# Performance work log

Hardware: AMD Instinct MI355X
Metric: run time of the kernel (lower is better)

Reference implementation:

```python
import jax, jax.numpy as jnp
import numpy as np

NEURONS = (3072, 8192, 8192, 10)
TSTEPS = 20
THRES = 1.0
DECAY = (2 ** 4 - 1) / 2 ** 4  # 0.9375


def setup_inputs() -> dict:
    key = jax.random.key(0)
    k_img, k1, k2, k3 = jax.random.split(key, 4)
    image = jax.random.uniform(k_img, (NEURONS[0],), dtype=jnp.float32)
    # He-style init matching torch.randn(neu_in, neu_out) * sqrt(2/neu_in)
    W1 = jax.random.normal(k1, (NEURONS[0], NEURONS[1]), dtype=jnp.float32) * np.sqrt(2 / NEURONS[0])
    W2 = jax.random.normal(k2, (NEURONS[1], NEURONS[2]), dtype=jnp.float32) * np.sqrt(2 / NEURONS[1])
    W3 = jax.random.normal(k3, (NEURONS[2], NEURONS[3]), dtype=jnp.float32) * np.sqrt(2 / NEURONS[2])
    return {"image": image, "W1": W1, "W2": W2, "W3": W3}


def _lif(m, spikes_in, W):
    # integrate: mempot += W.T @ spikes_in
    v = m + spikes_in @ W
    fire = (v >= THRES).astype(v.dtype)
    v = v - THRES * fire
    # leaky decay only where the neuron did not fire
    m_new = v * (fire + (1.0 - fire) * DECAY)
    return m_new, fire


def reference(image, W1, W2, W3):
    f32 = jnp.float32
    init = (
        jnp.zeros(NEURONS[0], f32),  # input membrane
        jnp.zeros(NEURONS[1], f32),  # lin1 membrane
        jnp.zeros(NEURONS[2], f32),  # lin2 membrane
        jnp.zeros(NEURONS[3], f32),  # lin3 membrane
        jnp.zeros(NEURONS[1], f32),  # lin1 spikes from previous step (spikes[t])
        jnp.zeros(NEURONS[2], f32),  # lin2 spikes from previous step
    )

    def step(state, _):
        mi, m1, m2, m3, s1_prev, s2_prev = state
        # input layer: integrate-and-fire, no decay
        mi = mi + image
        s_in = (mi >= THRES).astype(f32)
        mi = mi - THRES * s_in
        # lin1 sees input spikes of the SAME step; lin2/lin3 see previous-step
        # spikes of their pre-layer (pipeline delay in original loop)
        m1, s1 = _lif(m1, s_in, W1)
        m2, s2 = _lif(m2, s1_prev, W2)
        m3, s3 = _lif(m3, s2_prev, W3)
        return (mi, m1, m2, m3, s1, s2), s3

    _, s3_seq = jax.lax.scan(step, init, None, length=TSTEPS)
    # original stores lin3 spikes at indices 1..TSTEPS; index 0 stays zero
    spikes_out = jnp.concatenate([jnp.zeros((1, NEURONS[3]), f32), s3_seq], axis=0)
    return spikes_out
```

## Files before the change

kernel.cpp:

```cpp
#include <hip/hip_runtime.h>

#define TSTEPS 20
#define THRESV 1.0f
#define DECAYV 0.9375f

typedef float f32x4 __attribute__((ext_vector_type(4)));
typedef float f32x2 __attribute__((ext_vector_type(2)));

__device__ float g_sum1[TSTEPS][8192];
__device__ float g_sum2[TSTEPS][8192];
__device__ float g_sum3[TSTEPS][16];

__device__ unsigned g_mask1[3072];
__device__ float g_part1[32][20][8192];
__device__ unsigned g_mask2[8192];
__device__ float g_part2[64][19][8192];


__global__ void snn_input_kernel(const float* __restrict__ image,
                                 unsigned long long* __restrict__ s_in_bits) {
    int i = blockIdx.x * 256 + threadIdx.x;
    float img = image[i];
    float mi = 0.f;
    int word = i >> 6, lane = i & 63;
    for (int t = 0; t < TSTEPS; ++t) {
        mi += img;
        bool fire = (mi >= THRESV);
        if (fire) mi -= THRESV;
        unsigned long long bm = __ballot(fire);
        if (lane == 0) s_in_bits[t * 48 + word] = bm;
    }
}

struct __align__(16) SMem {
    unsigned short list[8192];
    float partials[512];
    unsigned long long bw[128];
    unsigned pc[128];
    int cntp;
};

template <int NW>
__device__ __forceinline__ int compact_par(const unsigned long long* bits, SMem& sm) {
    int tid = threadIdx.x;
    if (tid < NW) {
        unsigned long long w = bits[tid];
        sm.bw[tid] = w;
        sm.pc[tid] = (unsigned)__popcll(w);
    }
    __syncthreads();
    constexpr int WPW = NW / 8;
    int wave = tid >> 6, lane = tid & 63;
    int w0 = wave * WPW;
    int base = 0;
    for (int i = lane; i < w0; i += 64) base += (int)sm.pc[i];
    #pragma unroll
    for (int off = 1; off < 64; off <<= 1) base += __shfl_xor(base, off);
    if (wave == 0) {
        int tot = 0;
        for (int i = lane; i < NW; i += 64) tot += (int)sm.pc[i];
        #pragma unroll
        for (int off = 1; off < 64; off <<= 1) tot += __shfl_xor(tot, off);
        if (lane == 0) sm.cntp = tot;
    }
    for (int i = 0; i < WPW; ++i) {
        unsigned long long w = sm.bw[w0 + i];
        if ((w >> lane) & 1ull) {
            int pos = base + __popcll(w & ((1ull << lane) - 1ull));
            sm.list[pos] = (unsigned short)(((w0 + i) << 6) + lane);
        }
        base += __popcll(w);
    }
    __syncthreads();
    return sm.cntp;
}

#define GLD2(dst, ptr) \
    asm volatile("global_load_dwordx2 %0, %1, off" : "=v"(dst) : "v"(ptr))
#define WAIT8(a0,a1,a2,a3,a4,a5,a6,a7) \
    asm volatile("s_waitcnt vmcnt(0)" \
        : "+v"(a0),"+v"(a1),"+v"(a2),"+v"(a3),"+v"(a4),"+v"(a5),"+v"(a6),"+v"(a7))

__global__ void __launch_bounds__(512)
build_mask1_kernel(const unsigned long long* __restrict__ s_in_bits) {
    int i = blockIdx.x * 512 + threadIdx.x;
    if (i < 3072) {
        unsigned m = 0;
        #pragma unroll
        for (int t = 0; t < 20; ++t)
            m |= (unsigned)((s_in_bits[(size_t)t * 48 + (i >> 6)] >> (i & 63)) & 1ull) << t;
        g_mask1[i] = m;
    }
}

__device__ __forceinline__ void accrow20(f32x2 w, unsigned m, float* ax, float* ay) {
    #pragma unroll
    for (int bb = 0; bb < 20; ++bb)
        if (m & (1u << bb)) { ax[bb] += w.x; ay[bb] += w.y; }
}

__global__ void __launch_bounds__(512)
w1_dense_kernel(const float* __restrict__ W1) {
    __shared__ unsigned msk[96];
    int blk = blockIdx.x;
    int cs = blk >> 5;
    int rb = blk & 31;
    int tid = threadIdx.x;
    if (tid < 96) msk[tid] = g_mask1[rb * 96 + tid];
    __syncthreads();
    int j = cs * 1024 + tid * 2;
    const float* Wp = W1 + (size_t)rb * 96 * 8192 + j;
    float ax[20], ay[20];
    #pragma unroll
    for (int b = 0; b < 20; ++b) { ax[b] = 0.f; ay[b] = 0.f; }
    for (int r = 0; r < 96; r += 8) {
        const float* p = Wp + (size_t)r * 8192;
        f32x2 w0, w1, w2, w3, w4, w5, w6, w7;
        GLD2(w0, p);                GLD2(w1, p + 8192);
        GLD2(w2, p + 2 * 8192);     GLD2(w3, p + 3 * 8192);
        GLD2(w4, p + 4 * 8192);     GLD2(w5, p + 5 * 8192);
        GLD2(w6, p + 6 * 8192);     GLD2(w7, p + 7 * 8192);
        WAIT8(w0, w1, w2, w3, w4, w5, w6, w7);
        accrow20(w0, __builtin_amdgcn_readfirstlane(msk[r    ]), ax, ay);
        accrow20(w1, __builtin_amdgcn_readfirstlane(msk[r + 1]), ax, ay);
        accrow20(w2, __builtin_amdgcn_readfirstlane(msk[r + 2]), ax, ay);
        accrow20(w3, __builtin_amdgcn_readfirstlane(msk[r + 3]), ax, ay);
        accrow20(w4, __builtin_amdgcn_readfirstlane(msk[r + 4]), ax, ay);
        accrow20(w5, __builtin_amdgcn_readfirstlane(msk[r + 5]), ax, ay);
        accrow20(w6, __builtin_amdgcn_readfirstlane(msk[r + 6]), ax, ay);
        accrow20(w7, __builtin_amdgcn_readfirstlane(msk[r + 7]), ax, ay);
    }
    #pragma unroll
    for (int b = 0; b < 20; ++b)
        *(f32x2*)&g_part1[rb][b][j] = (f32x2){ax[b], ay[b]};
}

__global__ void __launch_bounds__(512)
w1_reduce_kernel() {
    int b = blockIdx.x;
    int t = b / 16;
    int j = (b % 16) * 512 + threadIdx.x;
    float s = 0.f;
    #pragma unroll 8
    for (int rb = 0; rb < 32; ++rb)
        s += g_part1[rb][t][j];
    g_sum1[t][j] = s;
}

__global__ void __launch_bounds__(512)
lif_chain_kernel(int which,
                 unsigned long long* __restrict__ bits_out,
                 int tstart) {
    const float* sums = (which == 0) ? &g_sum1[0][0] : &g_sum2[0][0];
    int j = blockIdx.x * 512 + threadIdx.x;
    int lane = threadIdx.x & 63;
    float m = 0.f;
    for (int t = tstart; t < TSTEPS; ++t) {
        float v = m + sums[(size_t)t * 8192 + j];
        bool fire = (v >= THRESV);
        if (fire) v -= THRESV;
        m = fire ? v : v * DECAYV;
        unsigned long long bm = __ballot(fire);
        if (lane == 0) bits_out[(size_t)t * 128 + (j >> 6)] = bm;
    }
}

__global__ void __launch_bounds__(512)
build_mask2_kernel(const unsigned long long* __restrict__ s1_bits) {
    int i = blockIdx.x * 512 + threadIdx.x;
    unsigned m = 0;
    #pragma unroll
    for (int b = 0; b < 19; ++b)
        m |= (unsigned)((s1_bits[(size_t)b * 128 + (i >> 6)] >> (i & 63)) & 1ull) << b;
    g_mask2[i] = m;
}

__device__ __forceinline__ void accrow(f32x2 w, unsigned m, float* ax, float* ay) {
    #pragma unroll
    for (int bb = 0; bb < 19; ++bb)
        if (m & (1u << bb)) { ax[bb] += w.x; ay[bb] += w.y; }
}

__global__ void __launch_bounds__(512)
w2_dense_kernel(const float* __restrict__ W2) {
    __shared__ unsigned msk[128];
    int blk = blockIdx.x;
    int cs = blk >> 6;
    int rb = blk & 63;
    int tid = threadIdx.x;
    if (tid < 128) msk[tid] = g_mask2[rb * 128 + tid];
    __syncthreads();
    int j = cs * 1024 + tid * 2;
    const float* Wp = W2 + (size_t)rb * 128 * 8192 + j;
    float ax[19], ay[19];
    #pragma unroll
    for (int b = 0; b < 19; ++b) { ax[b] = 0.f; ay[b] = 0.f; }
    for (int r = 0; r < 128; r += 8) {
        const float* p = Wp + (size_t)r * 8192;
        f32x2 w0, w1, w2, w3, w4, w5, w6, w7;
        GLD2(w0, p);                GLD2(w1, p + 8192);
        GLD2(w2, p + 2 * 8192);     GLD2(w3, p + 3 * 8192);
        GLD2(w4, p + 4 * 8192);     GLD2(w5, p + 5 * 8192);
        GLD2(w6, p + 6 * 8192);     GLD2(w7, p + 7 * 8192);
        WAIT8(w0, w1, w2, w3, w4, w5, w6, w7);
        accrow(w0, __builtin_amdgcn_readfirstlane(msk[r    ]), ax, ay);
        accrow(w1, __builtin_amdgcn_readfirstlane(msk[r + 1]), ax, ay);
        accrow(w2, __builtin_amdgcn_readfirstlane(msk[r + 2]), ax, ay);
        accrow(w3, __builtin_amdgcn_readfirstlane(msk[r + 3]), ax, ay);
        accrow(w4, __builtin_amdgcn_readfirstlane(msk[r + 4]), ax, ay);
        accrow(w5, __builtin_amdgcn_readfirstlane(msk[r + 5]), ax, ay);
        accrow(w6, __builtin_amdgcn_readfirstlane(msk[r + 6]), ax, ay);
        accrow(w7, __builtin_amdgcn_readfirstlane(msk[r + 7]), ax, ay);
    }
    #pragma unroll
    for (int b = 0; b < 19; ++b)
        *(f32x2*)&g_part2[rb][b][j] = (f32x2){ax[b], ay[b]};
}

__global__ void __launch_bounds__(512)
w2_reduce_kernel() {
    int b = blockIdx.x;
    int t = 1 + b / 16;
    int j = (b % 16) * 512 + threadIdx.x;
    float s = 0.f;
    #pragma unroll 8
    for (int rb = 0; rb < 64; ++rb)
        s += g_part2[rb][t - 1][j];
    g_sum2[t][j] = s;
}

__global__ void __launch_bounds__(512)
w3_sums_kernel(const float* __restrict__ W3,
               const unsigned long long* __restrict__ s2_bits) {
    __shared__ SMem sm;
    int t = blockIdx.x + 1;
    int tid = threadIdx.x;
    int count = compact_par<128>(s2_bits + (size_t)(t - 1) * 128, sm);
    int col = tid & 15, g = tid >> 4;
    float acc = 0.f;
    if (col < 10) {
        for (int k = g; k < count; k += 32)
            acc += W3[(size_t)sm.list[k] * 10 + col];
    }
    sm.partials[g * 16 + col] = acc;
    __syncthreads();
    if (tid < 10) {
        float s = 0.f;
        for (int gg = 0; gg < 32; ++gg) s += sm.partials[gg * 16 + tid];
        g_sum3[t][tid] = s;
    }
}

__global__ void w3_lif_kernel(float* __restrict__ out) {
    int tid = threadIdx.x;
    if (tid < 10) {
        float m = 0.f;
        for (int t = 1; t < TSTEPS; ++t) {
            float v = m + g_sum3[t][tid];
            bool fire = (v >= THRESV);
            if (fire) v -= THRESV;
            m = fire ? v : v * DECAYV;
            out[(t + 1) * 10 + tid] = fire ? 1.f : 0.f;
        }
    }
}

extern "C" void kernel_launch(void* const* d_in, const int* in_sizes, int n_in,
                              void* d_out, int out_size, void* d_ws, size_t ws_size,
                              hipStream_t stream) {
    const float* image = (const float*)d_in[0];
    const float* W1 = (const float*)d_in[1];
    const float* W2 = (const float*)d_in[2];
    const float* W3 = (const float*)d_in[3];
    float* out = (float*)d_out;

    char* ws = (char*)d_ws;
    unsigned long long* s_in_bits = (unsigned long long*)ws;
    unsigned long long* s1_bits = (unsigned long long*)(ws + 7680);
    unsigned long long* s2_bits = (unsigned long long*)(ws + 28160);

    hipMemsetAsync(d_ws, 0, 48640, stream);
    hipMemsetAsync(d_out, 0, (size_t)out_size * sizeof(float), stream);

    snn_input_kernel<<<12, 256, 0, stream>>>(image, s_in_bits);
    build_mask1_kernel<<<6, 512, 0, stream>>>(s_in_bits);
    w1_dense_kernel<<<8 * 32, 512, 0, stream>>>(W1);
    w1_reduce_kernel<<<20 * 16, 512, 0, stream>>>();
    lif_chain_kernel<<<16, 512, 0, stream>>>(0, s1_bits, 0);
    build_mask2_kernel<<<16, 512, 0, stream>>>(s1_bits);
    w2_dense_kernel<<<8 * 64, 512, 0, stream>>>(W2);
    w2_reduce_kernel<<<19 * 16, 512, 0, stream>>>();
    lif_chain_kernel<<<16, 512, 0, stream>>>(1, s2_bits, 1);
    w3_sums_kernel<<<TSTEPS - 1, 512, 0, stream>>>(W3, s2_bits);
    w3_lif_kernel<<<1, 64, 0, stream>>>(out);
}
```

Measured before the change: 177.6 us.

## Fuse mask building and partial reductions into LIF kernels, halve W2 row splits

The input kernel now writes the per-neuron spike masks directly, and the separate mask-building kernels are removed. The partial-sum reductions for layers 1 and 2 are folded into the LIF chain kernels, so the intermediate sum buffers go away. W2 is now split into 32 row blocks of 256 rows each instead of 64 blocks of 128, which halves the partial buffer traffic and halves the blocks launched for the W2 pass. The aim is fewer launches and less global memory traffic. The cost is that the LIF kernels, which run on only 16 blocks, now perform the reductions serially inside the time loop.

New measurement: 242.3 us. +36.4%, slower.

```diff
diff --git a/kernel.cpp b/kernel.cpp
--- a/kernel.cpp
+++ b/kernel.cpp
@@ -4,31 +4,30 @@
 #define THRESV 1.0f
 #define DECAYV 0.9375f
 
-typedef float f32x4 __attribute__((ext_vector_type(4)));
 typedef float f32x2 __attribute__((ext_vector_type(2)));
-
-__device__ float g_sum1[TSTEPS][8192];
-__device__ float g_sum2[TSTEPS][8192];
-__device__ float g_sum3[TSTEPS][16];
 
 __device__ unsigned g_mask1[3072];
 __device__ float g_part1[32][20][8192];
 __device__ unsigned g_mask2[8192];
-__device__ float g_part2[64][19][8192];
-
-
-__global__ void snn_input_kernel(const float* __restrict__ image,
-                                 unsigned long long* __restrict__ s_in_bits) {
-    int i = blockIdx.x * 256 + threadIdx.x;
-    float img = image[i];
-    float mi = 0.f;
-    int word = i >> 6, lane = i & 63;
-    for (int t = 0; t < TSTEPS; ++t) {
-        mi += img;
-        bool fire = (mi >= THRESV);
-        if (fire) mi -= THRESV;
-        unsigned long long bm = __ballot(fire);
-        if (lane == 0) s_in_bits[t * 48 + word] = bm;
+__device__ float g_part2[32][19][8192];
+__device__ float g_sum3[TSTEPS][16];
+
+
+__global__ void __launch_bounds__(512)
+snn_input_kernel(const float* __restrict__ image) {
+    int i = blockIdx.x * 512 + threadIdx.x;
+    if (i < 3072) {
+        float img = image[i];
+        float mi = 0.f;
+        unsigned mask = 0;
+        #pragma unroll
+        for (int t = 0; t < TSTEPS; ++t) {
+            mi += img;
+            bool fire = (mi >= THRESV);
+            if (fire) mi -= THRESV;
+            mask |= (unsigned)fire << t;
+        }
+        g_mask1[i] = mask;
     }
 }
 
@@ -80,18 +79,6 @@
 #define WAIT8(a0,a1,a2,a3,a4,a5,a6,a7) \
     asm volatile("s_waitcnt vmcnt(0)" \
         : "+v"(a0),"+v"(a1),"+v"(a2),"+v"(a3),"+v"(a4),"+v"(a5),"+v"(a6),"+v"(a7))
-
-__global__ void __launch_bounds__(512)
-build_mask1_kernel(const unsigned long long* __restrict__ s_in_bits) {
-    int i = blockIdx.x * 512 + threadIdx.x;
-    if (i < 3072) {
-        unsigned m = 0;
-        #pragma unroll
-        for (int t = 0; t < 20; ++t)
-            m |= (unsigned)((s_in_bits[(size_t)t * 48 + (i >> 6)] >> (i & 63)) & 1ull) << t;
-        g_mask1[i] = m;
-    }
-}
 
 __device__ __forceinline__ void accrow20(f32x2 w, unsigned m, float* ax, float* ay) {
     #pragma unroll
@@ -136,46 +123,24 @@
 }
 
 __global__ void __launch_bounds__(512)
-w1_reduce_kernel() {
-    int b = blockIdx.x;
-    int t = b / 16;
-    int j = (b % 16) * 512 + threadIdx.x;
-    float s = 0.f;
-    #pragma unroll 8
-    for (int rb = 0; rb < 32; ++rb)
-        s += g_part1[rb][t][j];
-    g_sum1[t][j] = s;
-}
-
-__global__ void __launch_bounds__(512)
-lif_chain_kernel(int which,
-                 unsigned long long* __restrict__ bits_out,
-                 int tstart) {
-    const float* sums = (which == 0) ? &g_sum1[0][0] : &g_sum2[0][0];
+lif1_kernel() {
     int j = blockIdx.x * 512 + threadIdx.x;
-    int lane = threadIdx.x & 63;
     float m = 0.f;
-    for (int t = tstart; t < TSTEPS; ++t) {
-        float v = m + sums[(size_t)t * 8192 + j];
+    unsigned mask = 0;
+    for (int t = 0; t < TSTEPS; ++t) {
+        float s = 0.f;
+        #pragma unroll 8
+        for (int rb = 0; rb < 32; ++rb) s += g_part1[rb][t][j];
+        float v = m + s;
         bool fire = (v >= THRESV);
         if (fire) v -= THRESV;
         m = fire ? v : v * DECAYV;
-        unsigned long long bm = __ballot(fire);
-        if (lane == 0) bits_out[(size_t)t * 128 + (j >> 6)] = bm;
-    }
-}
-
-__global__ void __launch_bounds__(512)
-build_mask2_kernel(const unsigned long long* __restrict__ s1_bits) {
-    int i = blockIdx.x * 512 + threadIdx.x;
-    unsigned m = 0;
-    #pragma unroll
-    for (int b = 0; b < 19; ++b)
-        m |= (unsigned)((s1_bits[(size_t)b * 128 + (i >> 6)] >> (i & 63)) & 1ull) << b;
-    g_mask2[i] = m;
-}
-
-__device__ __forceinline__ void accrow(f32x2 w, unsigned m, float* ax, float* ay) {
+        mask |= (unsigned)fire << t;
+    }
+    g_mask2[j] = mask;
+}
+
+__device__ __forceinline__ void accrow19(f32x2 w, unsigned m, float* ax, float* ay) {
     #pragma unroll
     for (int bb = 0; bb < 19; ++bb)
         if (m & (1u << bb)) { ax[bb] += w.x; ay[bb] += w.y; }
@@ -183,19 +148,19 @@
 
 __global__ void __launch_bounds__(512)
 w2_dense_kernel(const float* __restrict__ W2) {
-    __shared__ unsigned msk[128];
+    __shared__ unsigned msk[256];
     int blk = blockIdx.x;
-    int cs = blk >> 6;
-    int rb = blk & 63;
-    int tid = threadIdx.x;
-    if (tid < 128) msk[tid] = g_mask2[rb * 128 + tid];
+    int cs = blk >> 5;
+    int rb = blk & 31;
+    int tid = threadIdx.x;
+    if (tid < 256) msk[tid] = g_mask2[rb * 256 + tid];
     __syncthreads();
     int j = cs * 1024 + tid * 2;
-    const float* Wp = W2 + (size_t)rb * 128 * 8192 + j;
+    const float* Wp = W2 + (size_t)rb * 256 * 8192 + j;
     float ax[19], ay[19];
     #pragma unroll
     for (int b = 0; b < 19; ++b) { ax[b] = 0.f; ay[b] = 0.f; }
-    for (int r = 0; r < 128; r += 8) {
+    for (int r = 0; r < 256; r += 8) {
         const float* p = Wp + (size_t)r * 8192;
         f32x2 w0, w1, w2, w3, w4, w5, w6, w7;
         GLD2(w0, p);                GLD2(w1, p + 8192);
@@ -203,14 +168,14 @@
         GLD2(w4, p + 4 * 8192);     GLD2(w5, p + 5 * 8192);
         GLD2(w6, p + 6 * 8192);     GLD2(w7, p + 7 * 8192);
         WAIT8(w0, w1, w2, w3, w4, w5, w6, w7);
-        accrow(w0, __builtin_amdgcn_readfirstlane(msk[r    ]), ax, ay);
-        accrow(w1, __builtin_amdgcn_readfirstlane(msk[r + 1]), ax, ay);
-        accrow(w2, __builtin_amdgcn_readfirstlane(msk[r + 2]), ax, ay);
-        accrow(w3, __builtin_amdgcn_readfirstlane(msk[r + 3]), ax, ay);
-        accrow(w4, __builtin_amdgcn_readfirstlane(msk[r + 4]), ax, ay);
-        accrow(w5, __builtin_amdgcn_readfirstlane(msk[r + 5]), ax, ay);
-        accrow(w6, __builtin_amdgcn_readfirstlane(msk[r + 6]), ax, ay);
-        accrow(w7, __builtin_amdgcn_readfirstlane(msk[r + 7]), ax, ay);
+        accrow19(w0, __builtin_amdgcn_readfirstlane(msk[r    ]), ax, ay);
+        accrow19(w1, __builtin_amdgcn_readfirstlane(msk[r + 1]), ax, ay);
+        accrow19(w2, __builtin_amdgcn_readfirstlane(msk[r + 2]), ax, ay);
+        accrow19(w3, __builtin_amdgcn_readfirstlane(msk[r + 3]), ax, ay);
+        accrow19(w4, __builtin_amdgcn_readfirstlane(msk[r + 4]), ax, ay);
+        accrow19(w5, __builtin_amdgcn_readfirstlane(msk[r + 5]), ax, ay);
+        accrow19(w6, __builtin_amdgcn_readfirstlane(msk[r + 6]), ax, ay);
+        accrow19(w7, __builtin_amdgcn_readfirstlane(msk[r + 7]), ax, ay);
     }
     #pragma unroll
     for (int b = 0; b < 19; ++b)
@@ -218,15 +183,21 @@
 }
 
 __global__ void __launch_bounds__(512)
-w2_reduce_kernel() {
-    int b = blockIdx.x;
-    int t = 1 + b / 16;
-    int j = (b % 16) * 512 + threadIdx.x;
-    float s = 0.f;
-    #pragma unroll 8
-    for (int rb = 0; rb < 64; ++rb)
-        s += g_part2[rb][t - 1][j];
-    g_sum2[t][j] = s;
+lif2_kernel(unsigned long long* __restrict__ s2_bits) {
+    int j = blockIdx.x * 512 + threadIdx.x;
+    int lane = threadIdx.x & 63;
+    float m = 0.f;
+    for (int t = 1; t < TSTEPS; ++t) {
+        float s = 0.f;
+        #pragma unroll 8
+        for (int rb = 0; rb < 32; ++rb) s += g_part2[rb][t - 1][j];
+        float v = m + s;
+        bool fire = (v >= THRESV);
+        if (fire) v -= THRESV;
+        m = fire ? v : v * DECAYV;
+        unsigned long long bm = __ballot(fire);
+        if (lane == 0) s2_bits[(size_t)t * 128 + (j >> 6)] = bm;
+    }
 }
 
 __global__ void __launch_bounds__(512)
@@ -274,23 +245,16 @@
     const float* W3 = (const float*)d_in[3];
     float* out = (float*)d_out;
 
-    char* ws = (char*)d_ws;
-    unsigned long long* s_in_bits = (unsigned long long*)ws;
-    unsigned long long* s1_bits = (unsigned long long*)(ws + 7680);
-    unsigned long long* s2_bits = (unsigned long long*)(ws + 28160);
-
-    hipMemsetAsync(d_ws, 0, 48640, stream);
+    unsigned long long* s2_bits = (unsigned long long*)d_ws;
+
+    hipMemsetAsync(d_ws, 0, 20480, stream);
     hipMemsetAsync(d_out, 0, (size_t)out_size * sizeof(float), stream);
 
-    snn_input_kernel<<<12, 256, 0, stream>>>(image, s_in_bits);
-    build_mask1_kernel<<<6, 512, 0, stream>>>(s_in_bits);
+    snn_input_kernel<<<6, 512, 0, stream>>>(image);
     w1_dense_kernel<<<8 * 32, 512, 0, stream>>>(W1);
-    w1_reduce_kernel<<<20 * 16, 512, 0, stream>>>();
-    lif_chain_kernel<<<16, 512, 0, stream>>>(0, s1_bits, 0);
-    build_mask2_kernel<<<16, 512, 0, stream>>>(s1_bits);
-    w2_dense_kernel<<<8 * 64, 512, 0, stream>>>(W2);
-    w2_reduce_kernel<<<19 * 16, 512, 0, stream>>>();
-    lif_chain_kernel<<<16, 512, 0, stream>>>(1, s2_bits, 1);
+    lif1_kernel<<<16, 512, 0, stream>>>();
+    w2_dense_kernel<<<8 * 32, 512, 0, stream>>>(W2);
+    lif2_kernel<<<16, 512, 0, stream>>>(s2_bits);
     w3_sums_kernel<<<TSTEPS - 1, 512, 0, stream>>>(W3, s2_bits);
     w3_lif_kernel<<<1, 64, 0, stream>>>(out);
 }
```
